# Optimization experiments

Hardware: AMD Instinct MI355X
Metric: run time of the kernel (lower is better)

Reference implementation:

```python
import jax, jax.numpy as jnp
import numpy as np

N_E = 200000   # number of entities
N_T = 1000000  # number of KB triples
N_R = 200      # number of relations
N_W2V = 300    # question embedding dim
B = 64         # batch size


def _one_step(x, r, subj, rel, obj):
    # torch.sparse.mm(M_subj, x.T)      -> gather: x[:, subj]  (B, N_T)
    # torch.sparse.mm(M_rel.T, r.T)     -> gather: r[:, rel]   (B, N_T)
    # torch.sparse.mm(M_obj.T, x_t*r_t) -> scatter-add over obj ids
    m = x[:, subj] * r[:, rel]                                   # (B, N_T)
    x_new = jax.ops.segment_sum(m.T, obj, num_segments=N_E).T    # (B, N_E)
    return x_new


def setup_inputs() -> dict:
    key = jax.random.key(0)
    ks = jax.random.split(key, 11)
    x = jax.random.uniform(ks[0], (B, N_E), dtype=jnp.float32)
    q = jax.random.normal(ks[1], (B, N_W2V), dtype=jnp.float32)
    subj = jax.random.randint(ks[2], (N_T,), 0, N_E, dtype=jnp.int32)
    rel = jax.random.randint(ks[3], (N_T,), 0, N_R, dtype=jnp.int32)
    obj = jax.random.randint(ks[4], (N_T,), 0, N_E, dtype=jnp.int32)
    s = 1.0 / np.sqrt(N_W2V)  # nn.Linear default init scale
    W1 = jax.random.uniform(ks[5], (N_W2V, N_R), minval=-s, maxval=s, dtype=jnp.float32)
    b1 = jax.random.uniform(ks[6], (N_R,), minval=-s, maxval=s, dtype=jnp.float32)
    W2 = jax.random.uniform(ks[7], (N_W2V, N_R), minval=-s, maxval=s, dtype=jnp.float32)
    b2 = jax.random.uniform(ks[8], (N_R,), minval=-s, maxval=s, dtype=jnp.float32)
    W3 = jax.random.uniform(ks[9], (N_W2V, N_R), minval=-s, maxval=s, dtype=jnp.float32)
    b3 = jax.random.uniform(ks[10], (N_R,), minval=-s, maxval=s, dtype=jnp.float32)
    return {"x": x, "q": q, "W1": W1, "b1": b1, "W2": W2, "b2": b2,
            "W3": W3, "b3": b3, "subj": subj, "rel": rel, "obj": obj,
            "n_hop": 3}


def reference(x, q, W1, b1, W2, b2, W3, b3, subj, rel, obj, n_hop):
    layers = [(W1, b1), (W2, b2), (W3, b3)]
    for W, b in layers[:n_hop]:
        r = q @ W + b              # dense_i(q): (B, N_R)
        x = _one_step(x, r, subj, rel, obj)
    return x
```

## Files before the change

### kernel.cpp

```cpp
#include <hip/hip_runtime.h>
#include <hip/hip_fp16.h>

#define WAVE 64
#define NXCD 8
#define NRMAX 200
#define RSTRIDE 17
#define HOP_TPB 1024
#define HOP_BLOCKS 512
#define CSR_BLOCKS 2048
#define CSR_TPB 256
#define CAP 16
#define OVF_CAP 32768

__global__ void compute_r_kernel(const float* __restrict__ q,
                                 const float* __restrict__ W1, const float* __restrict__ b1,
                                 const float* __restrict__ W2, const float* __restrict__ b2,
                                 const float* __restrict__ W3, const float* __restrict__ b3,
                                 float* __restrict__ rT, int N_R, int N_W2V) {
    int lane = threadIdx.x & 63;
    int wv   = threadIdx.x >> 6;
    int b    = blockIdx.y * 4 + wv;
    int it   = blockIdx.x * 64 + lane;
    if (it >= 3 * N_R) return;
    int l = it / N_R;
    int j = it - l * N_R;
    const float* W  = (l == 0) ? W1 : (l == 1) ? W2 : W3;
    const float* bv = (l == 0) ? b1 : (l == 1) ? b2 : b3;
    const float* qrow = q + (size_t)b * N_W2V;
    float a0 = 0.f, a1 = 0.f, a2 = 0.f, a3 = 0.f;
    int k = 0;
    for (; k + 4 <= N_W2V; k += 4) {
        a0 = fmaf(qrow[k + 0], W[(size_t)(k + 0) * N_R + j], a0);
        a1 = fmaf(qrow[k + 1], W[(size_t)(k + 1) * N_R + j], a1);
        a2 = fmaf(qrow[k + 2], W[(size_t)(k + 2) * N_R + j], a2);
        a3 = fmaf(qrow[k + 3], W[(size_t)(k + 3) * N_R + j], a3);
    }
    for (; k < N_W2V; ++k)
        a0 = fmaf(qrow[k], W[(size_t)k * N_R + j], a0);
    rT[(size_t)it * WAVE + b] = bv[j] + ((a0 + a1) + (a2 + a3));
}

__global__ void transpose_in_f16_kernel(const float* __restrict__ in, __half2* __restrict__ out, int N_E) {
    __shared__ float tile[64][65];
    int e0 = blockIdx.x * 64;
    int li = threadIdx.x & 63;
    int lo = threadIdx.x >> 6;
    #pragma unroll
    for (int k = 0; k < 16; ++k) {
        int b = lo + 4 * k;
        int e = e0 + li;
        tile[b][li] = (e < N_E) ? in[(size_t)b * N_E + e] : 0.0f;
    }
    __syncthreads();
    #pragma unroll
    for (int k = 0; k < 8; ++k) {
        int idx = k * 256 + threadIdx.x;
        int ei  = idx >> 5;
        int j   = idx & 31;
        int e   = e0 + ei;
        if (e < N_E)
            out[(size_t)e * 32 + j] = __floats2half2_rn(tile[2 * j][ei], tile[2 * j + 1][ei]);
    }
}


__global__ void scatter_direct_kernel(const int* __restrict__ subj, const int* __restrict__ rel,
                                      const int* __restrict__ obj,
                                      int* __restrict__ cnt, unsigned* __restrict__ slots,
                                      int* __restrict__ novf, int* __restrict__ ovf_obj,
                                      unsigned* __restrict__ ovf_pk, int nT, int nE) {
    int grp = blockIdx.x & (NXCD - 1);
    int sh  = (nE + NXCD - 1) / NXCD;
    int lo  = grp * sh;
    int hi  = min(nE, lo + sh);
    int tid    = (blockIdx.x >> 3) * blockDim.x + threadIdx.x;
    int stride = (gridDim.x >> 3) * blockDim.x;
    int nT4 = nT >> 2;
    for (int t = tid; t < nT4; t += stride) {
        int4 o = ((const int4*)obj)[t];
        int base = t * 4;
        #pragma unroll
        for (int u = 0; u < 4; ++u) {
            int oo = (u == 0) ? o.x : (u == 1) ? o.y : (u == 2) ? o.z : o.w;
            if (oo >= lo && oo < hi) {
                unsigned pk = (unsigned)subj[base + u] | ((unsigned)rel[base + u] << 18);
                int slot = atomicAdd(&cnt[oo], 1);
                if (slot < CAP) slots[(size_t)oo * CAP + slot] = pk;
                else {
                    int oi = atomicAdd(novf, 1);
                    if (oi < OVF_CAP) { ovf_obj[oi] = oo; ovf_pk[oi] = pk; }
                }
            }
        }
    }
    for (int t = nT4 * 4 + tid; t < nT; t += stride) {
        int oo = obj[t];
        if (oo >= lo && oo < hi) {
            unsigned pk = (unsigned)subj[t] | ((unsigned)rel[t] << 18);
            int slot = atomicAdd(&cnt[oo], 1);
            if (slot < CAP) slots[(size_t)oo * CAP + slot] = pk;
            else {
                int oi = atomicAdd(novf, 1);
                if (oi < OVF_CAP) { ovf_obj[oi] = oo; ovf_pk[oi] = pk; }
            }
        }
    }
}


__device__ __forceinline__ float4 h4_to_f4(uint2 v) {
    float2 f0 = __half22float2(*(__half2*)&v.x);
    float2 f1 = __half22float2(*(__half2*)&v.y);
    return make_float4(f0.x, f0.y, f1.x, f1.y);
}

__device__ __forceinline__ uint2 pack_half4(float4 a) {
    __half2 h0 = __floats2half2_rn(a.x, a.y);
    __half2 h1 = __floats2half2_rn(a.z, a.w);
    uint2 v;
    v.x = *(unsigned*)&h0;
    v.y = *(unsigned*)&h1;
    return v;
}

__device__ __forceinline__ float4 hop_accum4(const uint2* __restrict__ xp,
                                             const float4* __restrict__ r_lds,
                                             const int* __restrict__ cnt,
                                             const unsigned* __restrict__ slots,
                                             int e, int g, int c, int nE) {
    float4 acc = make_float4(0.f, 0.f, 0.f, 0.f);
    int len = (e < nE) ? min(cnt[e], CAP) : 0;
    unsigned pv = (c < len) ? slots[(size_t)e * CAP + c] : 0u;
    int m = max(len, __shfl_xor(len, 16));
    m = max(m, __shfl_xor(m, 32));
    for (int j0 = 0; j0 < m; j0 += 8) {
        uint2 xv[8];
        unsigned pr[8];
        #pragma unroll
        for (int u = 0; u < 8; ++u) {
            int jj = max(min(j0 + u, len - 1), 0);
            unsigned p = __shfl(pv, (g << 4) + jj);
            pr[u] = p >> 18;
            xv[u] = xp[(size_t)(p & 0x3FFFFu) * 16 + c];
        }
        #pragma unroll
        for (int u = 0; u < 8; ++u) {
            if (j0 + u < len) {
                float4 rv = r_lds[pr[u] * RSTRIDE + c];
                float4 xf = h4_to_f4(xv[u]);
                acc.x = fmaf(xf.x, rv.x, acc.x);
                acc.y = fmaf(xf.y, rv.y, acc.y);
                acc.z = fmaf(xf.z, rv.z, acc.z);
                acc.w = fmaf(xf.w, rv.w, acc.w);
            }
        }
    }
    return acc;
}

__global__ __launch_bounds__(HOP_TPB, 8)
void hop_mid_kernel(const uint2* __restrict__ xp, const float4* __restrict__ rT4,
                    const int* __restrict__ cnt, const unsigned* __restrict__ slots,
                    uint2* __restrict__ yh, int nE, int nR) {
    __shared__ float4 r_lds[NRMAX * RSTRIDE];
    for (int i = threadIdx.x; i < nR * 16; i += HOP_TPB)
        r_lds[(i >> 4) * RSTRIDE + (i & 15)] = rT4[i];
    __syncthreads();
    int lane = threadIdx.x & 63;
    int g = lane >> 4, c = lane & 15;
    int wv = threadIdx.x >> 6;
    int nTiles = (nE + 63) >> 6;
    for (int t = blockIdx.x; t < nTiles; t += gridDim.x) {
        int e = t * 64 + wv * 4 + g;
        float4 acc = hop_accum4(xp, r_lds, cnt, slots, e, g, c, nE);
        if (e < nE) yh[(size_t)e * 16 + c] = pack_half4(acc);
    }
}

__global__ __launch_bounds__(HOP_TPB, 8)
void hop_out_kernel(const uint2* __restrict__ xp, const float4* __restrict__ rT4,
                    const int* __restrict__ cnt, const unsigned* __restrict__ slots,
                    float* __restrict__ out, int nE, int nR) {
    __shared__ float4 r_lds[NRMAX * RSTRIDE];
    __shared__ float tile[64][65];
    for (int i = threadIdx.x; i < nR * 16; i += HOP_TPB)
        r_lds[(i >> 4) * RSTRIDE + (i & 15)] = rT4[i];
    __syncthreads();
    int lane = threadIdx.x & 63;
    int g = lane >> 4, c = lane & 15;
    int wv = threadIdx.x >> 6;
    int nTiles = (nE + 63) >> 6;
    for (int t = blockIdx.x; t < nTiles; t += gridDim.x) {
        int e0 = t * 64;
        int ei = wv * 4 + g;
        float4 acc = hop_accum4(xp, r_lds, cnt, slots, e0 + ei, g, c, nE);
        tile[ei][4 * c + 0] = acc.x;
        tile[ei][4 * c + 1] = acc.y;
        tile[ei][4 * c + 2] = acc.z;
        tile[ei][4 * c + 3] = acc.w;
        __syncthreads();
        #pragma unroll
        for (int k = 0; k < 4; ++k) {
            int b = wv * 4 + k;
            int e = e0 + lane;
            if (e < nE) out[(size_t)b * nE + e] = tile[lane][b];
        }
        __syncthreads();
    }
}

__device__ __forceinline__ void atom_add_h2(unsigned* addr, float a, float b) {
    unsigned old = __atomic_load_n(addr, __ATOMIC_RELAXED), assumed;
    do {
        assumed = old;
        float2 f = __half22float2(*(__half2*)&assumed);
        __half2 nh = __floats2half2_rn(f.x + a, f.y + b);
        old = atomicCAS(addr, assumed, *(unsigned*)&nh);
    } while (old != assumed);
}

__global__ void ovf_mid_kernel(const uint2* __restrict__ xp, const float* __restrict__ rTl,
                               const int* __restrict__ novf, const int* __restrict__ ovf_obj,
                               const unsigned* __restrict__ ovf_pk, uint2* __restrict__ yh) {
    int n = min(*novf, OVF_CAP);
    int c = threadIdx.x & 15, grp = threadIdx.x >> 4;
    for (int i = blockIdx.x * 4 + grp; i < n; i += gridDim.x * 4) {
        int o = ovf_obj[i];
        unsigned p = ovf_pk[i];
        float4 xf = h4_to_f4(xp[(size_t)(p & 0x3FFFFu) * 16 + c]);
        const float* rr = rTl + (size_t)(p >> 18) * 64 + c * 4;
        unsigned* w = (unsigned*)&yh[(size_t)o * 16 + c];
        atom_add_h2(w,     xf.x * rr[0], xf.y * rr[1]);
        atom_add_h2(w + 1, xf.z * rr[2], xf.w * rr[3]);
    }
}

__global__ void ovf_out_kernel(const uint2* __restrict__ xp, const float* __restrict__ rTl,
                               const int* __restrict__ novf, const int* __restrict__ ovf_obj,
                               const unsigned* __restrict__ ovf_pk, float* __restrict__ out, int nE) {
    int n = min(*novf, OVF_CAP);
    int c = threadIdx.x & 15, grp = threadIdx.x >> 4;
    for (int i = blockIdx.x * 4 + grp; i < n; i += gridDim.x * 4) {
        int o = ovf_obj[i];
        unsigned p = ovf_pk[i];
        float4 xf = h4_to_f4(xp[(size_t)(p & 0x3FFFFu) * 16 + c]);
        const float* rr = rTl + (size_t)(p >> 18) * 64 + c * 4;
        atomicAdd(&out[(size_t)(4 * c + 0) * nE + o], xf.x * rr[0]);
        atomicAdd(&out[(size_t)(4 * c + 1) * nE + o], xf.y * rr[1]);
        atomicAdd(&out[(size_t)(4 * c + 2) * nE + o], xf.z * rr[2]);
        atomicAdd(&out[(size_t)(4 * c + 3) * nE + o], xf.w * rr[3]);
    }
}

extern "C" void kernel_launch(void* const* d_in, const int* in_sizes, int n_in,
                              void* d_out, int out_size, void* d_ws, size_t ws_size,
                              hipStream_t stream) {
    const float* x  = (const float*)d_in[0];
    const float* q  = (const float*)d_in[1];
    const float* W1 = (const float*)d_in[2];
    const float* b1 = (const float*)d_in[3];
    const float* W2 = (const float*)d_in[4];
    const float* b2 = (const float*)d_in[5];
    const float* W3 = (const float*)d_in[6];
    const float* b3 = (const float*)d_in[7];
    const int* subj = (const int*)d_in[8];
    const int* rel  = (const int*)d_in[9];
    const int* obj  = (const int*)d_in[10];

    const int B     = 64;
    const int N_E   = in_sizes[0] / B;
    const int N_W2V = in_sizes[1] / B;
    const int N_R   = in_sizes[3];
    const int N_T   = in_sizes[8];

    const size_t h16bytes = (size_t)N_E * B * sizeof(__half);

    int*      cnt     = (int*)d_ws;
    int*      novf    = cnt + N_E;
    int*      ovf_obj = novf + 4;
    unsigned* ovf_pk  = (unsigned*)(ovf_obj + OVF_CAP);
    unsigned* slots   = ovf_pk + OVF_CAP;
    char*     rT_raw  = (char*)(slots + (size_t)N_E * CAP);
    float*    rT      = (float*)(((uintptr_t)rT_raw + 15) & ~(uintptr_t)15);
    char*     X0      = (char*)(rT + (size_t)3 * N_R * B);
    size_t used = (size_t)(X0 - (char*)d_ws) + h16bytes;

    char* H1;
    if (ws_size >= used + h16bytes) {
        H1 = X0 + h16bytes;
        used += h16bytes;
    } else {
        H1 = (char*)d_out;
    }
    char* H2 = X0;

    {
        dim3 rgrid((3 * N_R + 63) / 64, B / 4);
        compute_r_kernel<<<rgrid, 256, 0, stream>>>(q, W1, b1, W2, b2, W3, b3, rT, N_R, N_W2V);
    }

    int tgrid = (N_E + 63) / 64;
    transpose_in_f16_kernel<<<tgrid, 256, 0, stream>>>(x, (__half2*)X0, N_E);

    hipMemsetAsync(cnt, 0, (size_t)(N_E + 4) * sizeof(int), stream);
    scatter_direct_kernel<<<CSR_BLOCKS, CSR_TPB, 0, stream>>>(
        subj, rel, obj, cnt, slots, novf, ovf_obj, ovf_pk, N_T, N_E);

    int nTiles  = (N_E + 63) / 64;
    int hblocks = nTiles < HOP_BLOCKS ? nTiles : HOP_BLOCKS;
    const float* rT1 = rT;
    const float* rT2 = rT + (size_t)1 * N_R * B;
    const float* rT3 = rT + (size_t)2 * N_R * B;

    hop_mid_kernel<<<hblocks, HOP_TPB, 0, stream>>>(
        (const uint2*)X0, (const float4*)rT1, cnt, slots, (uint2*)H1, N_E, N_R);
    ovf_mid_kernel<<<16, 64, 0, stream>>>(
        (const uint2*)X0, rT1, novf, ovf_obj, ovf_pk, (uint2*)H1);

    hop_mid_kernel<<<hblocks, HOP_TPB, 0, stream>>>(
        (const uint2*)H1, (const float4*)rT2, cnt, slots, (uint2*)H2, N_E, N_R);
    ovf_mid_kernel<<<16, 64, 0, stream>>>(
        (const uint2*)H1, rT2, novf, ovf_obj, ovf_pk, (uint2*)H2);

    hop_out_kernel<<<hblocks, HOP_TPB, 0, stream>>>(
        (const uint2*)H2, (const float4*)rT3, cnt, slots, (float*)d_out, N_E, N_R);
    ovf_out_kernel<<<16, 64, 0, stream>>>(
        (const uint2*)H2, rT3, novf, ovf_obj, ovf_pk, (float*)d_out, N_E);
}
```

Measured before the change: 354.1 us.

## Replace filtered scatter with two-pass binned partition then per-bin slot scatter

The single scatter kernel, in which every XCD group re-read all triples and kept only its own object range, becomes two passes. The first pass partitions triples into per-XCD, per-stripe regions using wave-level ballot aggregation. The second pass scatters each bin's entries into per-object slots. This removes the eightfold redundant reading of obj and keeps the per-object atomics local to one XCD's range. The cost is an extra kernel launch, roughly 1M packed entries written and read back through the region buffer, and more workspace.

```diff
diff --git a/kernel.cpp b/kernel.cpp
--- a/kernel.cpp
+++ b/kernel.cpp
@@ -11,6 +11,8 @@
 #define CSR_TPB 256
 #define CAP 16
 #define OVF_CAP 32768
+#define NSTRIPE 64
+#define REG_CAP 2304
 
 __global__ void compute_r_kernel(const float* __restrict__ q,
                                  const float* __restrict__ W1, const float* __restrict__ b1,
@@ -64,28 +66,36 @@
 }
 
 
-__global__ void scatter_direct_kernel(const int* __restrict__ subj, const int* __restrict__ rel,
-                                      const int* __restrict__ obj,
-                                      int* __restrict__ cnt, unsigned* __restrict__ slots,
-                                      int* __restrict__ novf, int* __restrict__ ovf_obj,
-                                      unsigned* __restrict__ ovf_pk, int nT, int nE) {
-    int grp = blockIdx.x & (NXCD - 1);
-    int sh  = (nE + NXCD - 1) / NXCD;
-    int lo  = grp * sh;
-    int hi  = min(nE, lo + sh);
-    int tid    = (blockIdx.x >> 3) * blockDim.x + threadIdx.x;
-    int stride = (gridDim.x >> 3) * blockDim.x;
-    int nT4 = nT >> 2;
-    for (int t = tid; t < nT4; t += stride) {
-        int4 o = ((const int4*)obj)[t];
-        int base = t * 4;
+__global__ void partition_kernel(const int* __restrict__ subj, const int* __restrict__ rel,
+                                 const int* __restrict__ obj,
+                                 int* __restrict__ bcur, uint2* __restrict__ regions,
+                                 int* __restrict__ novf, int* __restrict__ ovf_obj,
+                                 unsigned* __restrict__ ovf_pk, int nT, int nE) {
+    int sh = (nE + NXCD - 1) / NXCD;
+    int lane = threadIdx.x & 63;
+    int stripe = blockIdx.x & (NSTRIPE - 1);
+    int tid = blockIdx.x * blockDim.x + threadIdx.x;
+    int nw  = (gridDim.x * blockDim.x) >> 6;
+    int wid = tid >> 6;
+    for (long tb = (long)wid * 64; tb < nT; tb += (long)nw * 64) {
+        int t = (int)tb + lane;
+        bool v = t < nT;
+        int oo = v ? obj[t] : 0;
+        unsigned pk = v ? ((unsigned)subj[t] | ((unsigned)rel[t] << 18)) : 0u;
+        int b = v ? (oo / sh) : 8;
         #pragma unroll
-        for (int u = 0; u < 4; ++u) {
-            int oo = (u == 0) ? o.x : (u == 1) ? o.y : (u == 2) ? o.z : o.w;
-            if (oo >= lo && oo < hi) {
-                unsigned pk = (unsigned)subj[base + u] | ((unsigned)rel[base + u] << 18);
-                int slot = atomicAdd(&cnt[oo], 1);
-                if (slot < CAP) slots[(size_t)oo * CAP + slot] = pk;
+        for (int bin = 0; bin < 8; ++bin) {
+            unsigned long long m = __ballot(b == bin);
+            if (!m) continue;
+            int cnt_ = __popcll(m);
+            int leader = __ffsll((long long)m) - 1;
+            int base = 0;
+            if (lane == leader) base = atomicAdd(&bcur[bin * NSTRIPE + stripe], cnt_);
+            base = __shfl(base, leader);
+            if (b == bin) {
+                int off = base + __popcll(m & ((1ull << lane) - 1ull));
+                if (off < REG_CAP)
+                    regions[(size_t)(bin * NSTRIPE + stripe) * REG_CAP + off] = make_uint2((unsigned)oo, pk);
                 else {
                     int oi = atomicAdd(novf, 1);
                     if (oi < OVF_CAP) { ovf_obj[oi] = oo; ovf_pk[oi] = pk; }
@@ -93,16 +103,26 @@
             }
         }
     }
-    for (int t = nT4 * 4 + tid; t < nT; t += stride) {
-        int oo = obj[t];
-        if (oo >= lo && oo < hi) {
-            unsigned pk = (unsigned)subj[t] | ((unsigned)rel[t] << 18);
-            int slot = atomicAdd(&cnt[oo], 1);
-            if (slot < CAP) slots[(size_t)oo * CAP + slot] = pk;
-            else {
-                int oi = atomicAdd(novf, 1);
-                if (oi < OVF_CAP) { ovf_obj[oi] = oo; ovf_pk[oi] = pk; }
-            }
+}
+
+__global__ void scatter_bins_kernel(const int* __restrict__ bcur, const uint2* __restrict__ regions,
+                                    int* __restrict__ cnt, unsigned* __restrict__ slots,
+                                    int* __restrict__ novf, int* __restrict__ ovf_obj,
+                                    unsigned* __restrict__ ovf_pk) {
+    int g = blockIdx.x & (NXCD - 1);
+    int q = blockIdx.x >> 3;
+    int s = q & (NSTRIPE - 1);
+    int sub = q >> 6;
+    int n = min(bcur[g * NSTRIPE + s], REG_CAP);
+    const uint2* reg = regions + (size_t)(g * NSTRIPE + s) * REG_CAP;
+    for (int i = sub * blockDim.x + threadIdx.x; i < n; i += 4 * blockDim.x) {
+        uint2 e = reg[i];
+        int oo = (int)e.x;
+        int slot = atomicAdd(&cnt[oo], 1);
+        if (slot < CAP) slots[(size_t)oo * CAP + slot] = e.y;
+        else {
+            int oi = atomicAdd(novf, 1);
+            if (oi < OVF_CAP) { ovf_obj[oi] = oo; ovf_pk[oi] = e.y; }
         }
     }
 }
@@ -277,10 +297,12 @@
 
     int*      cnt     = (int*)d_ws;
     int*      novf    = cnt + N_E;
-    int*      ovf_obj = novf + 4;
+    int*      bcur    = novf + 4;
+    int*      ovf_obj = bcur + NXCD * NSTRIPE;
     unsigned* ovf_pk  = (unsigned*)(ovf_obj + OVF_CAP);
     unsigned* slots   = ovf_pk + OVF_CAP;
-    char*     rT_raw  = (char*)(slots + (size_t)N_E * CAP);
+    uint2*    regions = (uint2*)(slots + (size_t)N_E * CAP);
+    char*     rT_raw  = (char*)(regions + (size_t)NXCD * NSTRIPE * REG_CAP);
     float*    rT      = (float*)(((uintptr_t)rT_raw + 15) & ~(uintptr_t)15);
     char*     X0      = (char*)(rT + (size_t)3 * N_R * B);
     size_t used = (size_t)(X0 - (char*)d_ws) + h16bytes;
@@ -302,9 +324,11 @@
     int tgrid = (N_E + 63) / 64;
     transpose_in_f16_kernel<<<tgrid, 256, 0, stream>>>(x, (__half2*)X0, N_E);
 
-    hipMemsetAsync(cnt, 0, (size_t)(N_E + 4) * sizeof(int), stream);
-    scatter_direct_kernel<<<CSR_BLOCKS, CSR_TPB, 0, stream>>>(
-        subj, rel, obj, cnt, slots, novf, ovf_obj, ovf_pk, N_T, N_E);
+    hipMemsetAsync(cnt, 0, (size_t)(N_E + 4 + NXCD * NSTRIPE) * sizeof(int), stream);
+    partition_kernel<<<CSR_BLOCKS, CSR_TPB, 0, stream>>>(
+        subj, rel, obj, bcur, regions, novf, ovf_obj, ovf_pk, N_T, N_E);
+    scatter_bins_kernel<<<CSR_BLOCKS, CSR_TPB, 0, stream>>>(
+        bcur, regions, cnt, slots, novf, ovf_obj, ovf_pk);
 
     int nTiles  = (N_E + 63) / 64;
     int hblocks = nTiles < HOP_BLOCKS ? nTiles : HOP_BLOCKS;
```

New measurement: 470.8 us. 33.0% more time.
